# Kernel tuning notes

Hardware: AMD Instinct MI355X
Metric: run time of the kernel (lower is better)

## Reference

```python
import jax, jax.numpy as jnp
import numpy as np

D_EMBED = 512
NUM_HEADS = 8
HEAD_DIM = D_EMBED // NUM_HEADS
D_FF = 2048
B, L = 2, 4096
LN_EPS = 1e-5


def _layernorm(x, g, b):
    mu = jnp.mean(x, axis=-1, keepdims=True)
    var = jnp.mean(jnp.square(x - mu), axis=-1, keepdims=True)
    return (x - mu) * jax.lax.rsqrt(var + LN_EPS) * g + b


def setup_inputs() -> dict:
    key = jax.random.key(0)
    ks = jax.random.split(key, 16)
    s = 0.02
    inp = {
        "x": jax.random.normal(ks[0], (B, L, D_EMBED), dtype=jnp.float32),
        "mask": jnp.ones((B, 1, 1, L), dtype=jnp.int32),
        # attention projections (stored [in, out] for x @ W)
        "Wq": jax.random.normal(ks[1], (D_EMBED, D_EMBED), dtype=jnp.float32) * s,
        "bq": jnp.zeros((D_EMBED,), dtype=jnp.float32),
        "Wk": jax.random.normal(ks[2], (D_EMBED, D_EMBED), dtype=jnp.float32) * s,
        "bk": jnp.zeros((D_EMBED,), dtype=jnp.float32),
        "Wv": jax.random.normal(ks[3], (D_EMBED, D_EMBED), dtype=jnp.float32) * s,
        "bv": jnp.zeros((D_EMBED,), dtype=jnp.float32),
        "Wo": jax.random.normal(ks[4], (D_EMBED, D_EMBED), dtype=jnp.float32) * s,
        "bo": jnp.zeros((D_EMBED,), dtype=jnp.float32),
        # layernorms
        "ln1_g": jnp.ones((D_EMBED,), dtype=jnp.float32),
        "ln1_b": jnp.zeros((D_EMBED,), dtype=jnp.float32),
        "ln2_g": jnp.ones((D_EMBED,), dtype=jnp.float32),
        "ln2_b": jnp.zeros((D_EMBED,), dtype=jnp.float32),
        # FFN
        "W1": jax.random.normal(ks[5], (D_EMBED, D_FF), dtype=jnp.float32) * s,
        "b1": jnp.zeros((D_FF,), dtype=jnp.float32),
        "W2": jax.random.normal(ks[6], (D_FF, D_EMBED), dtype=jnp.float32) * s,
        "b2": jnp.zeros((D_EMBED,), dtype=jnp.float32),
    }
    return inp


def reference(x, mask, Wq, bq, Wk, bk, Wv, bv, Wo, bo, ln1_g, ln1_b,
              W1, b1, W2, b2, ln2_g, ln2_b):
    Bx, Lx, _ = x.shape
    # projections -> [B, H, L, Dh]
    def split_heads(t):
        return t.reshape(Bx, Lx, NUM_HEADS, HEAD_DIM).transpose(0, 2, 1, 3)
    q = split_heads(x @ Wq + bq)
    k = split_heads(x @ Wk + bk)
    v = split_heads(x @ Wv + bv)
    scores = jnp.einsum("bhqd,bhkd->bhqk", q, k) / jnp.sqrt(
        jnp.asarray(HEAD_DIM, dtype=x.dtype))
    scores = jnp.where(mask == 0, jnp.asarray(-1e9, dtype=x.dtype), scores)
    attn = jax.nn.softmax(scores, axis=-1)
    ctx = jnp.einsum("bhqk,bhkd->bhqd", attn, v)
    ctx = ctx.transpose(0, 2, 1, 3).reshape(Bx, Lx, D_EMBED)
    attn_out = ctx @ Wo + bo

    h = _layernorm(x + attn_out, ln1_g, ln1_b)
    ff = (jax.nn.gelu(h @ W1 + b1, approximate=False)) @ W2 + b2
    return _layernorm(h + ff, ln2_g, ln2_b)
```

## Files before the change

kernel.cpp:

```cpp
#include <hip/hip_runtime.h>
#include <hip/hip_bf16.h>
#include <math.h>

#define D_EMBED 512
#define NUM_HEADS 8
#define HEAD_DIM 64
#define D_FF 2048
#define BATCH 2
#define SEQ 4096
#define M_ROWS (BATCH*SEQ)
#define QSCALE 0.18033688011112042f

typedef __attribute__((ext_vector_type(8))) short short8;
typedef __attribute__((ext_vector_type(4))) short short4_t;
typedef __attribute__((ext_vector_type(4))) float f32x4;
typedef __attribute__((ext_vector_type(16))) float f32x16;

#if __has_builtin(__builtin_amdgcn_exp2f)
#define EXP2(x) __builtin_amdgcn_exp2f(x)
#else
#define EXP2(x) exp2f(x)
#endif

__device__ inline unsigned short f2b(float f) {
    union { float f; unsigned u; } v; v.f = f;
    unsigned r = v.u + 0x7fffu + ((v.u >> 16) & 1u);
    return (unsigned short)(r >> 16);
}

__device__ inline float b2f(short s) {
    union { unsigned u; float f; } v;
    v.u = ((unsigned)(unsigned short)s) << 16;
    return v.f;
}

__device__ inline short4_t pk4(float p0, float p1, float p2, float p3) {
    union { __hip_bfloat162 h2[2]; short4_t s4; } u;
    u.h2[0] = __float22bfloat162_rn(make_float2(p0, p1));
    u.h2[1] = __float22bfloat162_rn(make_float2(p2, p3));
    return u.s4;
}

__device__ inline unsigned pk2(float lo, float hi) {
    union { __hip_bfloat162 h2; unsigned u; } x;
    x.h2 = __float22bfloat162_rn(make_float2(lo, hi));
    return x.u;
}

__device__ inline void plswap(unsigned a, unsigned b, unsigned &r0, unsigned &r1) {
#if __has_builtin(__builtin_amdgcn_permlane32_swap)
    auto v = __builtin_amdgcn_permlane32_swap(a, b, false, false);
    r0 = (unsigned)v[0]; r1 = (unsigned)v[1];
#else
    unsigned ax = (unsigned)__shfl_xor((int)a, 32, 64);
    unsigned bx = (unsigned)__shfl_xor((int)b, 32, 64);
    bool hi = (threadIdx.x & 32) != 0;
    r0 = hi ? bx : a;
    r1 = hi ? b  : ax;
#endif
}

__device__ inline short8 pfrag8(const float* p) {
    unsigned a0 = pk2(p[0], p[1]), a1 = pk2(p[2], p[3]);
    unsigned b0 = pk2(p[4], p[5]), b1 = pk2(p[6], p[7]);
    unsigned u0, u1, u2, u3;
    plswap(a0, b0, u0, u1);
    plswap(a1, b1, u2, u3);
    union { unsigned u[4]; short8 s; } r;
    r.u[0] = u0; r.u[1] = u2; r.u[2] = u1; r.u[3] = u3;
    return r.s;
}

__device__ inline void gl2lds16(const void* g, void* l) {
    __builtin_amdgcn_global_load_lds(
        (const __attribute__((address_space(1))) unsigned int*)g,
        (__attribute__((address_space(3))) unsigned int*)l, 16, 0, 0);
}

template<int EPI>
__global__ __launch_bounds__(256) void gemm_bt(
    const unsigned short* __restrict__ A, const unsigned short* __restrict__ BT,
    const float* __restrict__ bias, void* __restrict__ Cout,
    int M, int N, int K)
{
    __shared__ __align__(16) unsigned short As[128*32];
    __shared__ __align__(16) unsigned short Bs[128*32];
    const int tid  = threadIdx.x;
    const int wave = tid >> 6, lane = tid & 63;
    const int wy = wave >> 1, wx = wave & 1;
    const int quad = lane >> 4, m16 = lane & 15;
    const int row0 = blockIdx.y * 128, n0 = blockIdx.x * 128;
    const int rdoff = (quad ^ ((m16 >> 1) & 3)) * 8;

    f32x4 acc[4][4];
#pragma unroll
    for (int i = 0; i < 4; i++)
#pragma unroll
        for (int j = 0; j < 4; j++) acc[i][j] = (f32x4){0.f,0.f,0.f,0.f};

    const int kIters = K >> 5;
    for (int kt = 0; kt < kIters; ++kt) {
        const int k0 = kt << 5;
#pragma unroll
        for (int it = 0; it < 2; ++it) {
            int g  = it*256 + tid;
            int r  = g >> 2;
            int c8 = (((g & 3) ^ ((g >> 3) & 3)) << 3);
            gl2lds16(A  + (size_t)(row0 + r)*K + k0 + c8, &As[(size_t)(it*256 + wave*64)*8]);
            gl2lds16(BT + (size_t)(n0  + r)*K + k0 + c8, &Bs[(size_t)(it*256 + wave*64)*8]);
        }
        __syncthreads();
        short8 a[4], b[4];
#pragma unroll
        for (int i = 0; i < 4; i++) a[i] = *(const short8*)&As[(wy*64 + i*16 + m16)*32 + rdoff];
#pragma unroll
        for (int j = 0; j < 4; j++) b[j] = *(const short8*)&Bs[(wx*64 + j*16 + m16)*32 + rdoff];
#pragma unroll
        for (int i = 0; i < 4; i++)
#pragma unroll
            for (int j = 0; j < 4; j++)
                acc[i][j] = __builtin_amdgcn_mfma_f32_16x16x32_bf16(a[i], b[j], acc[i][j], 0, 0, 0);
        __syncthreads();
    }

#pragma unroll
    for (int j = 0; j < 4; j++) {
        int col = n0 + wx*64 + j*16 + m16;
        float bj = bias[col];
#pragma unroll
        for (int i = 0; i < 4; i++) {
            int rbase = row0 + wy*64 + i*16 + quad*4;
#pragma unroll
            for (int r = 0; r < 4; r++) {
                float v = acc[i][j][r] + bj;
                size_t idx = (size_t)(rbase + r)*N + col;
                if (EPI == 0) {
                    ((unsigned short*)Cout)[idx] = f2b(v);
                } else {
                    float gv = 0.5f * v * (1.0f + erff(v * 0.70710678118654752f));
                    ((unsigned short*)Cout)[idx] = f2b(gv);
                }
            }
        }
    }
}

__global__ __launch_bounds__(256) void gemm_qkv(
    const unsigned short* __restrict__ A, const unsigned short* __restrict__ BT,
    const float* __restrict__ bias,
    unsigned short* __restrict__ Qp, unsigned short* __restrict__ Kp,
    unsigned short* __restrict__ Vp)
{
    const int K = 512;
    __shared__ __align__(16) unsigned short As[128*32];
    __shared__ __align__(16) unsigned short Bs[128*32];
    const int tid  = threadIdx.x;
    const int wave = tid >> 6, lane = tid & 63;
    const int wy = wave >> 1, wx = wave & 1;
    const int quad = lane >> 4, m16 = lane & 15;
    const int row0 = blockIdx.y * 128, n0 = blockIdx.x * 128;
    const int rdoff = (quad ^ ((m16 >> 1) & 3)) * 8;
    const int region = n0 >> 9;

    f32x4 acc[4][4];
#pragma unroll
    for (int i = 0; i < 4; i++)
#pragma unroll
        for (int j = 0; j < 4; j++) acc[i][j] = (f32x4){0.f,0.f,0.f,0.f};

    for (int kt = 0; kt < 16; ++kt) {
        const int k0 = kt << 5;
#pragma unroll
        for (int it = 0; it < 2; ++it) {
            int g  = it*256 + tid;
            int r  = g >> 2;
            int c8 = (((g & 3) ^ ((g >> 3) & 3)) << 3);
            gl2lds16(A  + (size_t)(row0 + r)*K + k0 + c8, &As[(size_t)(it*256 + wave*64)*8]);
            gl2lds16(BT + (size_t)(n0  + r)*K + k0 + c8, &Bs[(size_t)(it*256 + wave*64)*8]);
        }
        __syncthreads();
        short8 a[4], b[4];
#pragma unroll
        for (int i = 0; i < 4; i++) a[i] = *(const short8*)&As[(wy*64 + i*16 + m16)*32 + rdoff];
#pragma unroll
        for (int j = 0; j < 4; j++) b[j] = *(const short8*)&Bs[(wx*64 + j*16 + m16)*32 + rdoff];
#pragma unroll
        for (int i = 0; i < 4; i++)
#pragma unroll
            for (int j = 0; j < 4; j++)
                acc[i][j] = __builtin_amdgcn_mfma_f32_16x16x32_bf16(a[i], b[j], acc[i][j], 0, 0, 0);
        __syncthreads();
    }

    const float sc = (region == 0) ? QSCALE : 1.0f;
#pragma unroll
    for (int j = 0; j < 4; j++) {
        int col = n0 + wx*64 + j*16 + m16;
        float bj = bias[col];
        int cc = col & 511, h = cc >> 6, d = cc & 63;
#pragma unroll
        for (int i = 0; i < 4; i++) {
            int rbase = row0 + wy*64 + i*16 + quad*4;
#pragma unroll
            for (int r = 0; r < 4; r++) {
                float v = (acc[i][j][r] + bj) * sc;
                int row = rbase + r;
                int b = row >> 12, l = row & 4095;
                size_t bh = (size_t)(b*8 + h);
                if (region == 0) {
                    Qp[(bh*SEQ + l)*64 + d] = f2b(v);
                } else if (region == 1) {
                    Kp[(bh*SEQ + l)*64 + d] = f2b(v);
                } else {
                    Vp[(bh*64 + d)*SEQ + l] = f2b(v);
                }
            }
        }
    }
}

__global__ __launch_bounds__(256) void gemm_bt64(
    const unsigned short* __restrict__ A, const unsigned short* __restrict__ BT,
    const float* __restrict__ bias, unsigned short* __restrict__ Cout,
    int M, int N, int K)
{
    __shared__ __align__(16) unsigned short As[64*32];
    __shared__ __align__(16) unsigned short Bs[128*32];
    const int tid  = threadIdx.x;
    const int wave = tid >> 6, lane = tid & 63;
    const int wy = wave >> 1, wx = wave & 1;
    const int quad = lane >> 4, m16 = lane & 15;
    const int row0 = blockIdx.y * 64, n0 = blockIdx.x * 128;
    const int rdoff = (quad ^ ((m16 >> 1) & 3)) * 8;

    f32x4 acc[2][4];
#pragma unroll
    for (int i = 0; i < 2; i++)
#pragma unroll
        for (int j = 0; j < 4; j++) acc[i][j] = (f32x4){0.f,0.f,0.f,0.f};

    const int kIters = K >> 5;
    for (int kt = 0; kt < kIters; ++kt) {
        const int k0 = kt << 5;
        {
            int r = tid >> 2;
            int c8 = (((tid & 3) ^ ((tid >> 3) & 3)) << 3);
            gl2lds16(A + (size_t)(row0 + r)*K + k0 + c8, &As[(size_t)(wave*64)*8]);
        }
#pragma unroll
        for (int it = 0; it < 2; ++it) {
            int g  = it*256 + tid;
            int r  = g >> 2;
            int c8 = (((g & 3) ^ ((g >> 3) & 3)) << 3);
            gl2lds16(BT + (size_t)(n0 + r)*K + k0 + c8, &Bs[(size_t)(it*256 + wave*64)*8]);
        }
        __syncthreads();
        short8 a[2], b[4];
#pragma unroll
        for (int i = 0; i < 2; i++) a[i] = *(const short8*)&As[(wy*32 + i*16 + m16)*32 + rdoff];
#pragma unroll
        for (int j = 0; j < 4; j++) b[j] = *(const short8*)&Bs[(wx*64 + j*16 + m16)*32 + rdoff];
#pragma unroll
        for (int i = 0; i < 2; i++)
#pragma unroll
            for (int j = 0; j < 4; j++)
                acc[i][j] = __builtin_amdgcn_mfma_f32_16x16x32_bf16(a[i], b[j], acc[i][j], 0, 0, 0);
        __syncthreads();
    }

#pragma unroll
    for (int j = 0; j < 4; j++) {
        int col = n0 + wx*64 + j*16 + m16;
        float bj = bias[col];
#pragma unroll
        for (int i = 0; i < 2; i++) {
            int rbase = row0 + wy*32 + i*16 + quad*4;
#pragma unroll
            for (int r = 0; r < 4; r++) {
                float v = acc[i][j][r] + bj;
                Cout[(size_t)(rbase + r)*N + col] = f2b(v);
            }
        }
    }
}

__global__ __launch_bounds__(256) void prep(
    const float* __restrict__ Wq, const float* __restrict__ Wk,
    const float* __restrict__ Wv, const float* __restrict__ Wo,
    const float* __restrict__ W1, const float* __restrict__ W2,
    const float* __restrict__ bq, const float* __restrict__ bk,
    const float* __restrict__ bv, const int* __restrict__ mask,
    unsigned short* __restrict__ WqkvT, unsigned short* __restrict__ WoT,
    unsigned short* __restrict__ W1T, unsigned short* __restrict__ W2T,
    float* __restrict__ bqkv, int* __restrict__ mflag, unsigned* __restrict__ kmax2)
{
    const int id = blockIdx.x, t = threadIdx.x;
    if (id == 3072) {
        if (t < 64) {
            const int* m = mask + t*128;
            int all = 1;
            for (int i = 0; i < 128; i += 4) {
                int4 v = *(const int4*)(m + i);
                all &= (v.x && v.y && v.z && v.w) ? 1 : 0;
            }
            mflag[t] = all;
        }
        if (t < 16) kmax2[t] = 0u;
        for (int i = t; i < 1536; i += 256)
            bqkv[i] = (i < 512) ? bq[i] : ((i < 1024) ? bk[i-512] : bv[i-1024]);
        return;
    }
    __shared__ float tt[32][33];
    const float* W; unsigned short* WT; int K, N, bx, by;
    if (id < 256)       { W = Wq; WT = WqkvT;            K = 512;  N = 512;  bx = id & 15;  by = id >> 4; }
    else if (id < 512)  { int l = id - 256;  W = Wk; WT = WqkvT + 512*512;  K = 512;  N = 512;  bx = l & 15; by = l >> 4; }
    else if (id < 768)  { int l = id - 512;  W = Wv; WT = WqkvT + 1024*512; K = 512;  N = 512;  bx = l & 15; by = l >> 4; }
    else if (id < 1024) { int l = id - 768;  W = Wo; WT = WoT;              K = 512;  N = 512;  bx = l & 15; by = l >> 4; }
    else if (id < 2048) { int l = id - 1024; W = W1; WT = W1T;              K = 512;  N = 2048; bx = l & 63; by = l >> 6; }
    else                { int l = id - 2048; W = W2; WT = W2T;              K = 2048; N = 512;  bx = l & 15; by = l >> 4; }
    const int n0 = bx*32, k0 = by*32;
    const int x = t & 31, y = t >> 5;
#pragma unroll
    for (int yy = y; yy < 32; yy += 8) tt[yy][x] = W[(size_t)(k0+yy)*N + n0 + x];
    __syncthreads();
#pragma unroll
    for (int yy = y; yy < 32; yy += 8) WT[(size_t)(n0+yy)*K + k0 + x] = f2b(tt[x][yy]);
}

__global__ __launch_bounds__(256) void kmax_k(
    const unsigned short* __restrict__ Kp, unsigned* __restrict__ kmax2)
{
    const int bh = blockIdx.x, t = threadIdx.x;
    const int row = blockIdx.y*256 + t;
    const unsigned short* kp = Kp + ((size_t)bh*SEQ + row)*64;
    float s = 0.f;
#pragma unroll
    for (int c = 0; c < 8; ++c) {
        short8 v = *(const short8*)(kp + c*8);
#pragma unroll
        for (int j = 0; j < 8; ++j) { float f = b2f(v[j]); s += f*f; }
    }
#pragma unroll
    for (int off = 32; off >= 1; off >>= 1)
        s = fmaxf(s, __shfl_xor(s, off, 64));
    if ((t & 63) == 0) atomicMax(&kmax2[bh], __float_as_uint(s));
}

__global__ __launch_bounds__(512, 2) void flash_attn(
    const unsigned short* __restrict__ Qp, const unsigned short* __restrict__ Kp,
    const unsigned short* __restrict__ Vt, const int* __restrict__ mask,
    const int* __restrict__ flags, const unsigned* __restrict__ kmax2,
    unsigned short* __restrict__ O)
{
    __shared__ __align__(16) unsigned short Ks[2][128*64];
    __shared__ __align__(16) unsigned short Vs[2][64*128];
    __shared__ float rsh[4][2][64];
    const int tid = threadIdx.x, wave = tid >> 6, lane = tid & 63;
    const int qsub = wave & 3, parity = wave >> 2;
    const int c = lane & 31, l5 = lane >> 5;
    const int bh = blockIdx.y, b = bh >> 3, h = bh & 7;
    const int qbase = blockIdx.x * 256 + qsub * 64;

    const unsigned short* Qb = Qp + (size_t)bh*SEQ*64;
    const unsigned short* Kb = Kp + (size_t)bh*SEQ*64;
    const unsigned short* Vb = Vt + (size_t)bh*64*SEQ;
    const int* mbase = mask + b*SEQ;
    const int* fbase = flags + b*(SEQ/128);
    const float kmx = __uint_as_float(kmax2[bh]);

    short8 qf[2][4];
    float Mq[2];
#pragma unroll
    for (int qs = 0; qs < 2; ++qs) {
        const unsigned short* qp = Qb + (size_t)(qbase + qs*32 + c)*64 + l5*8;
        float qn2 = 0.f;
#pragma unroll
        for (int t = 0; t < 4; ++t) {
            qf[qs][t] = *(const short8*)(qp + t*16);
#pragma unroll
            for (int j = 0; j < 8; ++j) { float f = b2f(qf[qs][t][j]); qn2 += f*f; }
        }
        qn2 += __shfl_xor(qn2, 32, 64);
        Mq[qs] = sqrtf(qn2 * kmx);
    }

    f32x16 accO[2][2];
#pragma unroll
    for (int qs = 0; qs < 2; ++qs)
#pragma unroll
        for (int dg = 0; dg < 2; ++dg)
#pragma unroll
            for (int r = 0; r < 16; ++r) accO[qs][dg][r] = 0.f;
    float rs0 = 0.f, rs1 = 0.f;

#define STAGE(nb, ktn) do {                                                   \
        const int key0s = (ktn)*128;                                          \
        _Pragma("unroll")                                                     \
        for (int it = 0; it < 2; ++it) {                                      \
            int idx = it*512 + tid;                                           \
            int r = idx >> 3, chn = idx & 7;                                  \
            gl2lds16(Kb + (size_t)(key0s + r)*64 + ((chn ^ (r & 7)) << 3),    \
                     &Ks[nb][(it*512 + wave*64)*8]);                          \
        }                                                                     \
        _Pragma("unroll")                                                     \
        for (int it = 0; it < 2; ++it) {                                      \
            int idx = it*512 + tid;                                           \
            int r = idx >> 4, chn = idx & 15;                                 \
            gl2lds16(Vb + (size_t)r*SEQ + key0s + ((chn ^ (r & 15)) << 3),    \
                     &Vs[nb][(it*512 + wave*64)*8]);                          \
        }                                                                     \
    } while (0)

    STAGE(0, 0);
    __syncthreads();
    int cb = 0;
    const int NT = SEQ/128;

    for (int kt = 0; kt < NT; ++kt) {
        if (kt + 1 < NT) STAGE(cb ^ 1, kt + 1);
        const int allones = fbase[kt];
        const int key0 = kt * 128;
        const unsigned short* Kt  = Ks[cb];
        const unsigned short* Vtl = Vs[cb];

#pragma unroll
        for (int g = 0; g < 2; ++g) {
            const int kg = parity*2 + g;
            short8 kf[4];
#pragma unroll
            for (int t = 0; t < 4; ++t) {
                int row = kg*32 + c;
                int chn = (t*2 + l5) ^ (row & 7);
                kf[t] = *(const short8*)&Kt[row*64 + chn*8];
            }
            f32x16 s0, s1;
#pragma unroll
            for (int r = 0; r < 16; ++r) { s0[r] = -Mq[0]; s1[r] = -Mq[1]; }
#pragma unroll
            for (int t = 0; t < 4; ++t) {
                s0 = __builtin_amdgcn_mfma_f32_32x32x16_bf16(kf[t], qf[0][t], s0, 0, 0, 0);
                s1 = __builtin_amdgcn_mfma_f32_32x32x16_bf16(kf[t], qf[1][t], s1, 0, 0, 0);
            }
            if (!allones) {
#pragma unroll
                for (int r = 0; r < 16; ++r) {
                    int mv = mbase[key0 + kg*32 + (r & 3) + 8*(r >> 2) + 4*l5];
                    if (!mv) { s0[r] = -1e9f; s1[r] = -1e9f; }
                }
            }
            float pa[16], pc[16];
#pragma unroll
            for (int r = 0; r < 16; ++r) { pa[r] = EXP2(s0[r]); pc[r] = EXP2(s1[r]); }
            rs0 += (((pa[0]+pa[1])+(pa[2]+pa[3])) + ((pa[4]+pa[5])+(pa[6]+pa[7])))
                 + (((pa[8]+pa[9])+(pa[10]+pa[11])) + ((pa[12]+pa[13])+(pa[14]+pa[15])));
            rs1 += (((pc[0]+pc[1])+(pc[2]+pc[3])) + ((pc[4]+pc[5])+(pc[6]+pc[7])))
                 + (((pc[8]+pc[9])+(pc[10]+pc[11])) + ((pc[12]+pc[13])+(pc[14]+pc[15])));

            short8 vf[2][2];
#pragma unroll
            for (int c2 = 0; c2 < 2; ++c2)
#pragma unroll
                for (int dg = 0; dg < 2; ++dg) {
                    int row = dg*32 + c;
                    int chn = ((kg*2 + c2)*2 + l5) ^ (row & 15);
                    vf[c2][dg] = *(const short8*)&Vtl[row*128 + chn*8];
                }
#pragma unroll
            for (int c2 = 0; c2 < 2; ++c2) {
                short8 pf0 = pfrag8(&pa[c2*8]);
                short8 pf1 = pfrag8(&pc[c2*8]);
                accO[0][0] = __builtin_amdgcn_mfma_f32_32x32x16_bf16(vf[c2][0], pf0, accO[0][0], 0, 0, 0);
                accO[0][1] = __builtin_amdgcn_mfma_f32_32x32x16_bf16(vf[c2][1], pf0, accO[0][1], 0, 0, 0);
                accO[1][0] = __builtin_amdgcn_mfma_f32_32x32x16_bf16(vf[c2][0], pf1, accO[1][0], 0, 0, 0);
                accO[1][1] = __builtin_amdgcn_mfma_f32_32x32x16_bf16(vf[c2][1], pf1, accO[1][1], 0, 0, 0);
            }
        }
        __syncthreads();
        cb ^= 1;
    }
#undef STAGE

    float* mp = (qsub < 2) ? ((float*)&Ks[0][0] + qsub*4096)
                           : ((float*)&Vs[0][0] + (qsub - 2)*4096);
    if (parity) {
#pragma unroll
        for (int qs = 0; qs < 2; ++qs)
#pragma unroll
            for (int dg = 0; dg < 2; ++dg)
#pragma unroll
                for (int r = 0; r < 16; ++r)
                    mp[(qs*2 + dg)*1024 + r*64 + lane] = accO[qs][dg][r];
        rsh[qsub][0][lane] = rs0;
        rsh[qsub][1][lane] = rs1;
    }
    __syncthreads();
    if (!parity) {
#pragma unroll
        for (int qs = 0; qs < 2; ++qs)
#pragma unroll
            for (int dg = 0; dg < 2; ++dg)
#pragma unroll
                for (int r = 0; r < 16; ++r)
                    accO[qs][dg][r] += mp[(qs*2 + dg)*1024 + r*64 + lane];
        rs0 += rsh[qsub][0][lane];
        rs1 += rsh[qsub][1][lane];

        rs0 += __shfl_xor(rs0, 32, 64);
        rs1 += __shfl_xor(rs1, 32, 64);
        float rl[2] = { 1.0f/rs0, 1.0f/rs1 };
#pragma unroll
        for (int qs = 0; qs < 2; ++qs) {
            int qrow = qbase + qs*32 + c;
            unsigned short* op = O + (size_t)(b*SEQ + qrow)*D_EMBED + h*HEAD_DIM;
#pragma unroll
            for (int dg = 0; dg < 2; ++dg)
#pragma unroll
                for (int q4 = 0; q4 < 4; ++q4) {
                    short4_t o = pk4(accO[qs][dg][q4*4+0]*rl[qs], accO[qs][dg][q4*4+1]*rl[qs],
                                     accO[qs][dg][q4*4+2]*rl[qs], accO[qs][dg][q4*4+3]*rl[qs]);
                    *(short4_t*)&op[dg*32 + q4*8 + l5*4] = o;
                }
        }
    }
}

__global__ __launch_bounds__(256) void ln_res1(
    const float* __restrict__ A, const unsigned short* __restrict__ Bv,
    const float* __restrict__ g, const float* __restrict__ be,
    unsigned short* __restrict__ Yb)
{
    const int wave = threadIdx.x >> 6, lane = threadIdx.x & 63;
    const int row = blockIdx.x * 4 + wave;
    const float* ap = A + (size_t)row*512 + lane*8;
    short8 bv = *(const short8*)(Bv + (size_t)row*512 + lane*8);
    float v[8]; float s = 0.f;
#pragma unroll
    for (int j = 0; j < 8; j++) { v[j] = ap[j] + b2f(bv[j]); s += v[j]; }
#pragma unroll
    for (int off = 32; off >= 1; off >>= 1) s += __shfl_xor(s, off, 64);
    float mu = s * (1.f/512.f);
    float q = 0.f;
#pragma unroll
    for (int j = 0; j < 8; j++) { v[j] -= mu; q += v[j]*v[j]; }
#pragma unroll
    for (int off = 32; off >= 1; off >>= 1) q += __shfl_xor(q, off, 64);
    float rstd = rsqrtf(q * (1.f/512.f) + 1e-5f);
#pragma unroll
    for (int j = 0; j < 8; j++) {
        float y = v[j]*rstd*g[lane*8+j] + be[lane*8+j];
        Yb[(size_t)row*512 + lane*8 + j] = f2b(y);
    }
}

__global__ __launch_bounds__(256) void ln_res2(
    const unsigned short* __restrict__ A, const unsigned short* __restrict__ Bv,
    const float* __restrict__ g, const float* __restrict__ be,
    float* __restrict__ Yf)
{
    const int wave = threadIdx.x >> 6, lane = threadIdx.x & 63;
    const int row = blockIdx.x * 4 + wave;
    short8 av = *(const short8*)(A  + (size_t)row*512 + lane*8);
    short8 bv = *(const short8*)(Bv + (size_t)row*512 + lane*8);
    float v[8]; float s = 0.f;
#pragma unroll
    for (int j = 0; j < 8; j++) { v[j] = b2f(av[j]) + b2f(bv[j]); s += v[j]; }
#pragma unroll
    for (int off = 32; off >= 1; off >>= 1) s += __shfl_xor(s, off, 64);
    float mu = s * (1.f/512.f);
    float q = 0.f;
#pragma unroll
    for (int j = 0; j < 8; j++) { v[j] -= mu; q += v[j]*v[j]; }
#pragma unroll
    for (int off = 32; off >= 1; off >>= 1) q += __shfl_xor(q, off, 64);
    float rstd = rsqrtf(q * (1.f/512.f) + 1e-5f);
#pragma unroll
    for (int j = 0; j < 8; j++) {
        float y = v[j]*rstd*g[lane*8+j] + be[lane*8+j];
        Yf[(size_t)row*512 + lane*8 + j] = y;
    }
}

__global__ __launch_bounds__(256) void cvt_f32_bf16(
    const float* __restrict__ X, unsigned short* __restrict__ Y, int n)
{
    int idx = (blockIdx.x * 256 + threadIdx.x) * 4;
    if (idx < n) {
        float4 v = *(const float4*)(X + idx);
        Y[idx+0] = f2b(v.x); Y[idx+1] = f2b(v.y);
        Y[idx+2] = f2b(v.z); Y[idx+3] = f2b(v.w);
    }
}

extern "C" void kernel_launch(void* const* d_in, const int* in_sizes, int n_in,
                              void* d_out, int out_size, void* d_ws, size_t ws_size,
                              hipStream_t stream)
{
    const float* x    = (const float*)d_in[0];
    const int*   mask = (const int*)  d_in[1];
    const float* Wq = (const float*)d_in[2];  const float* bq = (const float*)d_in[3];
    const float* Wk = (const float*)d_in[4];  const float* bk = (const float*)d_in[5];
    const float* Wv = (const float*)d_in[6];  const float* bv = (const float*)d_in[7];
    const float* Wo = (const float*)d_in[8];  const float* bo = (const float*)d_in[9];
    const float* ln1g = (const float*)d_in[10]; const float* ln1b = (const float*)d_in[11];
    const float* ln2g = (const float*)d_in[12]; const float* ln2b = (const float*)d_in[13];
    const float* W1 = (const float*)d_in[14]; const float* b1 = (const float*)d_in[15];
    const float* W2 = (const float*)d_in[16]; const float* b2 = (const float*)d_in[17];
    float* out = (float*)d_out;

    char* ws = (char*)d_ws;
    const size_t MB = 1024*1024;
    unsigned short* xb    = (unsigned short*)(ws + 0);
    unsigned short* WqkvT = (unsigned short*)(ws + 8*MB);
    unsigned short* W1T   = (unsigned short*)(ws + 10*MB);
    unsigned short* W2T   = (unsigned short*)(ws + 12*MB);
    unsigned short* WoT   = (unsigned short*)(ws + 14*MB);
    float*          bqkv  = (float*)(ws + 14*MB + 512*1024);
    int*            mflag = (int*)(ws + 14*MB + 768*1024);
    unsigned*       kmaxb = (unsigned*)(ws + 14*MB + 772*1024);
    unsigned short* Qp    = (unsigned short*)(ws + 15*MB);
    unsigned short* Kp    = (unsigned short*)(ws + 23*MB);
    unsigned short* Vp    = (unsigned short*)(ws + 31*MB);
    unsigned short* ctx   = (unsigned short*)(ws + 39*MB);
    unsigned short* atfb  = (unsigned short*)(ws + 47*MB);
    unsigned short* hb    = (unsigned short*)(ws + 0);
    unsigned short* Gb    = (unsigned short*)(ws + 15*MB);
    unsigned short* ffb   = (unsigned short*)(ws + 47*MB);

    cvt_f32_bf16<<<4096, 256, 0, stream>>>(x, xb, M_ROWS*D_EMBED);
    prep<<<3073, 256, 0, stream>>>(Wq, Wk, Wv, Wo, W1, W2, bq, bk, bv, mask,
                                   WqkvT, WoT, W1T, W2T, bqkv, mflag, kmaxb);

    gemm_qkv<<<dim3(12,64), 256, 0, stream>>>(xb, WqkvT, bqkv, Qp, Kp, Vp);

    kmax_k<<<dim3(16,16), 256, 0, stream>>>(Kp, kmaxb);
    flash_attn<<<dim3(SEQ/256, 16), 512, 0, stream>>>(Qp, Kp, Vp, mask, mflag, kmaxb, ctx);

    gemm_bt64<<<dim3(4,128), 256, 0, stream>>>(ctx, WoT, bo, atfb, M_ROWS, 512, 512);
    ln_res1<<<M_ROWS/4, 256, 0, stream>>>(x, atfb, ln1g, ln1b, hb);

    gemm_bt<2><<<dim3(16,64), 256, 0, stream>>>(hb, W1T, b1, Gb, M_ROWS, D_FF, 512);
    gemm_bt64<<<dim3(4,128), 256, 0, stream>>>(Gb, W2T, b2, ffb, M_ROWS, 512, D_FF);
    ln_res2<<<M_ROWS/4, 256, 0, stream>>>(hb, ffb, ln2g, ln2b, out);
}
```

Baseline: 346.1 us.

## Split flash-attention key tiles across four wave groups with 128-query blocks

Each block now covers 128 queries with 2 query-subgroups of waves and 4 key-partition waves per 128-key tile, instead of 256 queries with 2 key partitions. This doubles the grid to 512 blocks to improve CU fill, and raises the launch-bounds occupancy hint to 4 blocks. The cost is that each K/V tile loaded into LDS is reused by half as many queries, so global K/V traffic doubles, and the final cross-wave reduction of accumulators and row sums now takes two LDS merge rounds with extra barriers. The tighter launch bound may also cap registers and risk spills.

```diff
diff --git a/kernel.cpp b/kernel.cpp
--- a/kernel.cpp
+++ b/kernel.cpp
@@ -346,7 +346,7 @@
     if ((t & 63) == 0) atomicMax(&kmax2[bh], __float_as_uint(s));
 }
 
-__global__ __launch_bounds__(512, 2) void flash_attn(
+__global__ __launch_bounds__(512, 4) void flash_attn(
     const unsigned short* __restrict__ Qp, const unsigned short* __restrict__ Kp,
     const unsigned short* __restrict__ Vt, const int* __restrict__ mask,
     const int* __restrict__ flags, const unsigned* __restrict__ kmax2,
@@ -354,12 +354,12 @@
 {
     __shared__ __align__(16) unsigned short Ks[2][128*64];
     __shared__ __align__(16) unsigned short Vs[2][64*128];
-    __shared__ float rsh[4][2][64];
+    __shared__ float rsp[8][2][64];
     const int tid = threadIdx.x, wave = tid >> 6, lane = tid & 63;
-    const int qsub = wave & 3, parity = wave >> 2;
+    const int qsub = wave & 1, kp = wave >> 1;
     const int c = lane & 31, l5 = lane >> 5;
     const int bh = blockIdx.y, b = bh >> 3, h = bh & 7;
-    const int qbase = blockIdx.x * 256 + qsub * 64;
+    const int qbase = blockIdx.x * 128 + qsub * 64;
 
     const unsigned short* Qb = Qp + (size_t)bh*SEQ*64;
     const unsigned short* Kb = Kp + (size_t)bh*SEQ*64;
@@ -422,88 +422,112 @@
         const int key0 = kt * 128;
         const unsigned short* Kt  = Ks[cb];
         const unsigned short* Vtl = Vs[cb];
-
-#pragma unroll
-        for (int g = 0; g < 2; ++g) {
-            const int kg = parity*2 + g;
-            short8 kf[4];
-#pragma unroll
-            for (int t = 0; t < 4; ++t) {
-                int row = kg*32 + c;
-                int chn = (t*2 + l5) ^ (row & 7);
-                kf[t] = *(const short8*)&Kt[row*64 + chn*8];
+        const int kg = kp;
+
+        short8 kf[4];
+#pragma unroll
+        for (int t = 0; t < 4; ++t) {
+            int row = kg*32 + c;
+            int chn = (t*2 + l5) ^ (row & 7);
+            kf[t] = *(const short8*)&Kt[row*64 + chn*8];
+        }
+        f32x16 s0, s1;
+#pragma unroll
+        for (int r = 0; r < 16; ++r) { s0[r] = -Mq[0]; s1[r] = -Mq[1]; }
+#pragma unroll
+        for (int t = 0; t < 4; ++t) {
+            s0 = __builtin_amdgcn_mfma_f32_32x32x16_bf16(kf[t], qf[0][t], s0, 0, 0, 0);
+            s1 = __builtin_amdgcn_mfma_f32_32x32x16_bf16(kf[t], qf[1][t], s1, 0, 0, 0);
+        }
+        if (!allones) {
+#pragma unroll
+            for (int r = 0; r < 16; ++r) {
+                int mv = mbase[key0 + kg*32 + (r & 3) + 8*(r >> 2) + 4*l5];
+                if (!mv) { s0[r] = -1e9f; s1[r] = -1e9f; }
             }
-            f32x16 s0, s1;
-#pragma unroll
-            for (int r = 0; r < 16; ++r) { s0[r] = -Mq[0]; s1[r] = -Mq[1]; }
-#pragma unroll
-            for (int t = 0; t < 4; ++t) {
-                s0 = __builtin_amdgcn_mfma_f32_32x32x16_bf16(kf[t], qf[0][t], s0, 0, 0, 0);
-                s1 = __builtin_amdgcn_mfma_f32_32x32x16_bf16(kf[t], qf[1][t], s1, 0, 0, 0);
+        }
+        float pa[16], pc[16];
+#pragma unroll
+        for (int r = 0; r < 16; ++r) { pa[r] = EXP2(s0[r]); pc[r] = EXP2(s1[r]); }
+        rs0 += (((pa[0]+pa[1])+(pa[2]+pa[3])) + ((pa[4]+pa[5])+(pa[6]+pa[7])))
+             + (((pa[8]+pa[9])+(pa[10]+pa[11])) + ((pa[12]+pa[13])+(pa[14]+pa[15])));
+        rs1 += (((pc[0]+pc[1])+(pc[2]+pc[3])) + ((pc[4]+pc[5])+(pc[6]+pc[7])))
+             + (((pc[8]+pc[9])+(pc[10]+pc[11])) + ((pc[12]+pc[13])+(pc[14]+pc[15])));
+
+        short8 vf[2][2];
+#pragma unroll
+        for (int c2 = 0; c2 < 2; ++c2)
+#pragma unroll
+            for (int dg = 0; dg < 2; ++dg) {
+                int row = dg*32 + c;
+                int chn = ((kg*2 + c2)*2 + l5) ^ (row & 15);
+                vf[c2][dg] = *(const short8*)&Vtl[row*128 + chn*8];
             }
-            if (!allones) {
-#pragma unroll
-                for (int r = 0; r < 16; ++r) {
-                    int mv = mbase[key0 + kg*32 + (r & 3) + 8*(r >> 2) + 4*l5];
-                    if (!mv) { s0[r] = -1e9f; s1[r] = -1e9f; }
-                }
-            }
-            float pa[16], pc[16];
-#pragma unroll
-            for (int r = 0; r < 16; ++r) { pa[r] = EXP2(s0[r]); pc[r] = EXP2(s1[r]); }
-            rs0 += (((pa[0]+pa[1])+(pa[2]+pa[3])) + ((pa[4]+pa[5])+(pa[6]+pa[7])))
-                 + (((pa[8]+pa[9])+(pa[10]+pa[11])) + ((pa[12]+pa[13])+(pa[14]+pa[15])));
-            rs1 += (((pc[0]+pc[1])+(pc[2]+pc[3])) + ((pc[4]+pc[5])+(pc[6]+pc[7])))
-                 + (((pc[8]+pc[9])+(pc[10]+pc[11])) + ((pc[12]+pc[13])+(pc[14]+pc[15])));
-
-            short8 vf[2][2];
-#pragma unroll
-            for (int c2 = 0; c2 < 2; ++c2)
-#pragma unroll
-                for (int dg = 0; dg < 2; ++dg) {
-                    int row = dg*32 + c;
-                    int chn = ((kg*2 + c2)*2 + l5) ^ (row & 15);
-                    vf[c2][dg] = *(const short8*)&Vtl[row*128 + chn*8];
-                }
-#pragma unroll
-            for (int c2 = 0; c2 < 2; ++c2) {
-                short8 pf0 = pfrag8(&pa[c2*8]);
-                short8 pf1 = pfrag8(&pc[c2*8]);
-                accO[0][0] = __builtin_amdgcn_mfma_f32_32x32x16_bf16(vf[c2][0], pf0, accO[0][0], 0, 0, 0);
-                accO[0][1] = __builtin_amdgcn_mfma_f32_32x32x16_bf16(vf[c2][1], pf0, accO[0][1], 0, 0, 0);
-                accO[1][0] = __builtin_amdgcn_mfma_f32_32x32x16_bf16(vf[c2][0], pf1, accO[1][0], 0, 0, 0);
-                accO[1][1] = __builtin_amdgcn_mfma_f32_32x32x16_bf16(vf[c2][1], pf1, accO[1][1], 0, 0, 0);
-            }
-        }
+#pragma unroll
+        for (int c2 = 0; c2 < 2; ++c2) {
+            short8 pf0 = pfrag8(&pa[c2*8]);
+            short8 pf1 = pfrag8(&pc[c2*8]);
+            accO[0][0] = __builtin_amdgcn_mfma_f32_32x32x16_bf16(vf[c2][0], pf0, accO[0][0], 0, 0, 0);
+            accO[0][1] = __builtin_amdgcn_mfma_f32_32x32x16_bf16(vf[c2][1], pf0, accO[0][1], 0, 0, 0);
+            accO[1][0] = __builtin_amdgcn_mfma_f32_32x32x16_bf16(vf[c2][0], pf1, accO[1][0], 0, 0, 0);
+            accO[1][1] = __builtin_amdgcn_mfma_f32_32x32x16_bf16(vf[c2][1], pf1, accO[1][1], 0, 0, 0);
+        }
+
         __syncthreads();
         cb ^= 1;
     }
 #undef STAGE
 
-    float* mp = (qsub < 2) ? ((float*)&Ks[0][0] + qsub*4096)
-                           : ((float*)&Vs[0][0] + (qsub - 2)*4096);
-    if (parity) {
+    float* const ksf = (float*)&Ks[0][0];
+    float* const vsf = (float*)&Vs[0][0];
+    rsp[wave][0][lane] = rs0;
+    rsp[wave][1][lane] = rs1;
+    if (kp >= 2) {
+        int s = (kp - 2)*2 + qsub;
+        float* mp = (s < 2) ? ksf + s*4096 : vsf + (s - 2)*4096;
 #pragma unroll
         for (int qs = 0; qs < 2; ++qs)
 #pragma unroll
             for (int dg = 0; dg < 2; ++dg)
 #pragma unroll
                 for (int r = 0; r < 16; ++r)
-                    mp[(qs*2 + dg)*1024 + r*64 + lane] = accO[qs][dg][r];
-        rsh[qsub][0][lane] = rs0;
-        rsh[qsub][1][lane] = rs1;
+                    mp[((qs*2 + dg)*16 + r)*64 + lane] = accO[qs][dg][r];
     }
     __syncthreads();
-    if (!parity) {
+    if (kp < 2) {
+        int s = kp*2 + qsub;
+        float* mp = (s < 2) ? ksf + s*4096 : vsf + (s - 2)*4096;
 #pragma unroll
         for (int qs = 0; qs < 2; ++qs)
 #pragma unroll
             for (int dg = 0; dg < 2; ++dg)
 #pragma unroll
                 for (int r = 0; r < 16; ++r)
-                    accO[qs][dg][r] += mp[(qs*2 + dg)*1024 + r*64 + lane];
-        rs0 += rsh[qsub][0][lane];
-        rs1 += rsh[qsub][1][lane];
+                    accO[qs][dg][r] += mp[((qs*2 + dg)*16 + r)*64 + lane];
+    }
+    __syncthreads();
+    if (kp == 1) {
+        float* mp = ksf + qsub*4096;
+#pragma unroll
+        for (int qs = 0; qs < 2; ++qs)
+#pragma unroll
+            for (int dg = 0; dg < 2; ++dg)
+#pragma unroll
+                for (int r = 0; r < 16; ++r)
+                    mp[((qs*2 + dg)*16 + r)*64 + lane] = accO[qs][dg][r];
+    }
+    __syncthreads();
+    if (kp == 0) {
+        float* mp = ksf + qsub*4096;
+#pragma unroll
+        for (int qs = 0; qs < 2; ++qs)
+#pragma unroll
+            for (int dg = 0; dg < 2; ++dg)
+#pragma unroll
+                for (int r = 0; r < 16; ++r)
+                    accO[qs][dg][r] += mp[((qs*2 + dg)*16 + r)*64 + lane];
+        rs0 += rsp[2 + qsub][0][lane] + rsp[4 + qsub][0][lane] + rsp[6 + qsub][0][lane];
+        rs1 += rsp[2 + qsub][1][lane] + rsp[4 + qsub][1][lane] + rsp[6 + qsub][1][lane];
 
         rs0 += __shfl_xor(rs0, 32, 64);
         rs1 += __shfl_xor(rs1, 32, 64);
@@ -633,7 +657,7 @@
     gemm_qkv<<<dim3(12,64), 256, 0, stream>>>(xb, WqkvT, bqkv, Qp, Kp, Vp);
 
     kmax_k<<<dim3(16,16), 256, 0, stream>>>(Kp, kmaxb);
-    flash_attn<<<dim3(SEQ/256, 16), 512, 0, stream>>>(Qp, Kp, Vp, mask, mflag, kmaxb, ctx);
+    flash_attn<<<dim3(SEQ/128, 16), 512, 0, stream>>>(Qp, Kp, Vp, mask, mflag, kmaxb, ctx);
 
     gemm_bt64<<<dim3(4,128), 256, 0, stream>>>(ctx, WoT, bo, atfb, M_ROWS, 512, 512);
     ln_res1<<<M_ROWS/4, 256, 0, stream>>>(x, atfb, ln1g, ln1b, hb);
```

Measured after the change: 793.8 us. 2.29x slower.

## Halve queries per wave in flash attention to double grid occupancy

Applied to the files above, without the earlier changes.

Each wave in the flash attention kernel now processes 32 query rows instead of 64, so a block covers 128 queries and the grid doubles. This aims to give each CU more resident blocks and waves, improving latency hiding and load balance across CUs. The trade-off is that each K/V tile is loaded and staged into LDS for half as many queries, doubling K/V global and LDS traffic per unit of work. Register pressure per wave drops because the accumulators halve.

```diff
diff --git a/kernel.cpp b/kernel.cpp
--- a/kernel.cpp
+++ b/kernel.cpp
@@ -354,12 +354,12 @@
 {
     __shared__ __align__(16) unsigned short Ks[2][128*64];
     __shared__ __align__(16) unsigned short Vs[2][64*128];
-    __shared__ float rsh[4][2][64];
+    __shared__ float rsp[8][64];
     const int tid = threadIdx.x, wave = tid >> 6, lane = tid & 63;
-    const int qsub = wave & 3, parity = wave >> 2;
+    const int qsub = wave & 3, kp = wave >> 2;
     const int c = lane & 31, l5 = lane >> 5;
     const int bh = blockIdx.y, b = bh >> 3, h = bh & 7;
-    const int qbase = blockIdx.x * 256 + qsub * 64;
+    const int qbase = blockIdx.x * 128 + qsub * 32;
 
     const unsigned short* Qb = Qp + (size_t)bh*SEQ*64;
     const unsigned short* Kb = Kp + (size_t)bh*SEQ*64;
@@ -368,30 +368,27 @@
     const int* fbase = flags + b*(SEQ/128);
     const float kmx = __uint_as_float(kmax2[bh]);
 
-    short8 qf[2][4];
-    float Mq[2];
-#pragma unroll
-    for (int qs = 0; qs < 2; ++qs) {
-        const unsigned short* qp = Qb + (size_t)(qbase + qs*32 + c)*64 + l5*8;
+    short8 qf[4];
+    float Mq;
+    {
+        const unsigned short* qp = Qb + (size_t)(qbase + c)*64 + l5*8;
         float qn2 = 0.f;
 #pragma unroll
         for (int t = 0; t < 4; ++t) {
-            qf[qs][t] = *(const short8*)(qp + t*16);
-#pragma unroll
-            for (int j = 0; j < 8; ++j) { float f = b2f(qf[qs][t][j]); qn2 += f*f; }
+            qf[t] = *(const short8*)(qp + t*16);
+#pragma unroll
+            for (int j = 0; j < 8; ++j) { float f = b2f(qf[t][j]); qn2 += f*f; }
         }
         qn2 += __shfl_xor(qn2, 32, 64);
-        Mq[qs] = sqrtf(qn2 * kmx);
-    }
-
-    f32x16 accO[2][2];
-#pragma unroll
-    for (int qs = 0; qs < 2; ++qs)
-#pragma unroll
-        for (int dg = 0; dg < 2; ++dg)
-#pragma unroll
-            for (int r = 0; r < 16; ++r) accO[qs][dg][r] = 0.f;
-    float rs0 = 0.f, rs1 = 0.f;
+        Mq = sqrtf(qn2 * kmx);
+    }
+
+    f32x16 accO[2];
+#pragma unroll
+    for (int dg = 0; dg < 2; ++dg)
+#pragma unroll
+        for (int r = 0; r < 16; ++r) accO[dg][r] = 0.f;
+    float rs = 0.f;
 
 #define STAGE(nb, ktn) do {                                                   \
         const int key0s = (ktn)*128;                                          \
@@ -425,7 +422,7 @@
 
 #pragma unroll
         for (int g = 0; g < 2; ++g) {
-            const int kg = parity*2 + g;
+            const int kg = kp*2 + g;
             short8 kf[4];
 #pragma unroll
             for (int t = 0; t < 4; ++t) {
@@ -433,28 +430,24 @@
                 int chn = (t*2 + l5) ^ (row & 7);
                 kf[t] = *(const short8*)&Kt[row*64 + chn*8];
             }
-            f32x16 s0, s1;
-#pragma unroll
-            for (int r = 0; r < 16; ++r) { s0[r] = -Mq[0]; s1[r] = -Mq[1]; }
-#pragma unroll
-            for (int t = 0; t < 4; ++t) {
-                s0 = __builtin_amdgcn_mfma_f32_32x32x16_bf16(kf[t], qf[0][t], s0, 0, 0, 0);
-                s1 = __builtin_amdgcn_mfma_f32_32x32x16_bf16(kf[t], qf[1][t], s1, 0, 0, 0);
-            }
+            f32x16 s;
+#pragma unroll
+            for (int r = 0; r < 16; ++r) s[r] = -Mq;
+#pragma unroll
+            for (int t = 0; t < 4; ++t)
+                s = __builtin_amdgcn_mfma_f32_32x32x16_bf16(kf[t], qf[t], s, 0, 0, 0);
             if (!allones) {
 #pragma unroll
                 for (int r = 0; r < 16; ++r) {
                     int mv = mbase[key0 + kg*32 + (r & 3) + 8*(r >> 2) + 4*l5];
-                    if (!mv) { s0[r] = -1e9f; s1[r] = -1e9f; }
+                    if (!mv) s[r] = -1e9f;
                 }
             }
-            float pa[16], pc[16];
-#pragma unroll
-            for (int r = 0; r < 16; ++r) { pa[r] = EXP2(s0[r]); pc[r] = EXP2(s1[r]); }
-            rs0 += (((pa[0]+pa[1])+(pa[2]+pa[3])) + ((pa[4]+pa[5])+(pa[6]+pa[7])))
-                 + (((pa[8]+pa[9])+(pa[10]+pa[11])) + ((pa[12]+pa[13])+(pa[14]+pa[15])));
-            rs1 += (((pc[0]+pc[1])+(pc[2]+pc[3])) + ((pc[4]+pc[5])+(pc[6]+pc[7])))
-                 + (((pc[8]+pc[9])+(pc[10]+pc[11])) + ((pc[12]+pc[13])+(pc[14]+pc[15])));
+            float pa[16];
+#pragma unroll
+            for (int r = 0; r < 16; ++r) pa[r] = EXP2(s[r]);
+            rs += (((pa[0]+pa[1])+(pa[2]+pa[3])) + ((pa[4]+pa[5])+(pa[6]+pa[7])))
+                + (((pa[8]+pa[9])+(pa[10]+pa[11])) + ((pa[12]+pa[13])+(pa[14]+pa[15])));
 
             short8 vf[2][2];
 #pragma unroll
@@ -467,12 +460,9 @@
                 }
 #pragma unroll
             for (int c2 = 0; c2 < 2; ++c2) {
-                short8 pf0 = pfrag8(&pa[c2*8]);
-                short8 pf1 = pfrag8(&pc[c2*8]);
-                accO[0][0] = __builtin_amdgcn_mfma_f32_32x32x16_bf16(vf[c2][0], pf0, accO[0][0], 0, 0, 0);
-                accO[0][1] = __builtin_amdgcn_mfma_f32_32x32x16_bf16(vf[c2][1], pf0, accO[0][1], 0, 0, 0);
-                accO[1][0] = __builtin_amdgcn_mfma_f32_32x32x16_bf16(vf[c2][0], pf1, accO[1][0], 0, 0, 0);
-                accO[1][1] = __builtin_amdgcn_mfma_f32_32x32x16_bf16(vf[c2][1], pf1, accO[1][1], 0, 0, 0);
+                short8 pf = pfrag8(&pa[c2*8]);
+                accO[0] = __builtin_amdgcn_mfma_f32_32x32x16_bf16(vf[c2][0], pf, accO[0], 0, 0, 0);
+                accO[1] = __builtin_amdgcn_mfma_f32_32x32x16_bf16(vf[c2][1], pf, accO[1], 0, 0, 0);
             }
         }
         __syncthreads();
@@ -480,47 +470,37 @@
     }
 #undef STAGE
 
-    float* mp = (qsub < 2) ? ((float*)&Ks[0][0] + qsub*4096)
-                           : ((float*)&Vs[0][0] + (qsub - 2)*4096);
-    if (parity) {
-#pragma unroll
-        for (int qs = 0; qs < 2; ++qs)
-#pragma unroll
-            for (int dg = 0; dg < 2; ++dg)
-#pragma unroll
-                for (int r = 0; r < 16; ++r)
-                    mp[(qs*2 + dg)*1024 + r*64 + lane] = accO[qs][dg][r];
-        rsh[qsub][0][lane] = rs0;
-        rsh[qsub][1][lane] = rs1;
+    float* const ksf = (float*)&Ks[0][0];
+    rsp[wave][lane] = rs;
+    float* mp = ksf + qsub*2048;
+    if (kp == 1) {
+#pragma unroll
+        for (int dg = 0; dg < 2; ++dg)
+#pragma unroll
+            for (int r = 0; r < 16; ++r)
+                mp[(dg*16 + r)*64 + lane] = accO[dg][r];
     }
     __syncthreads();
-    if (!parity) {
-#pragma unroll
-        for (int qs = 0; qs < 2; ++qs)
-#pragma unroll
-            for (int dg = 0; dg < 2; ++dg)
-#pragma unroll
-                for (int r = 0; r < 16; ++r)
-                    accO[qs][dg][r] += mp[(qs*2 + dg)*1024 + r*64 + lane];
-        rs0 += rsh[qsub][0][lane];
-        rs1 += rsh[qsub][1][lane];
-
-        rs0 += __shfl_xor(rs0, 32, 64);
-        rs1 += __shfl_xor(rs1, 32, 64);
-        float rl[2] = { 1.0f/rs0, 1.0f/rs1 };
-#pragma unroll
-        for (int qs = 0; qs < 2; ++qs) {
-            int qrow = qbase + qs*32 + c;
-            unsigned short* op = O + (size_t)(b*SEQ + qrow)*D_EMBED + h*HEAD_DIM;
-#pragma unroll
-            for (int dg = 0; dg < 2; ++dg)
-#pragma unroll
-                for (int q4 = 0; q4 < 4; ++q4) {
-                    short4_t o = pk4(accO[qs][dg][q4*4+0]*rl[qs], accO[qs][dg][q4*4+1]*rl[qs],
-                                     accO[qs][dg][q4*4+2]*rl[qs], accO[qs][dg][q4*4+3]*rl[qs]);
-                    *(short4_t*)&op[dg*32 + q4*8 + l5*4] = o;
-                }
-        }
+    if (kp == 0) {
+#pragma unroll
+        for (int dg = 0; dg < 2; ++dg)
+#pragma unroll
+            for (int r = 0; r < 16; ++r)
+                accO[dg][r] += mp[(dg*16 + r)*64 + lane];
+        rs += rsp[4 + qsub][lane];
+
+        rs += __shfl_xor(rs, 32, 64);
+        float rl = 1.0f / rs;
+        int qrow = qbase + c;
+        unsigned short* op = O + (size_t)(b*SEQ + qrow)*D_EMBED + h*HEAD_DIM;
+#pragma unroll
+        for (int dg = 0; dg < 2; ++dg)
+#pragma unroll
+            for (int q4 = 0; q4 < 4; ++q4) {
+                short4_t o = pk4(accO[dg][q4*4+0]*rl, accO[dg][q4*4+1]*rl,
+                                 accO[dg][q4*4+2]*rl, accO[dg][q4*4+3]*rl);
+                *(short4_t*)&op[dg*32 + q4*8 + l5*4] = o;
+            }
     }
 }
 
@@ -633,7 +613,7 @@
     gemm_qkv<<<dim3(12,64), 256, 0, stream>>>(xb, WqkvT, bqkv, Qp, Kp, Vp);
 
     kmax_k<<<dim3(16,16), 256, 0, stream>>>(Kp, kmaxb);
-    flash_attn<<<dim3(SEQ/256, 16), 512, 0, stream>>>(Qp, Kp, Vp, mask, mflag, kmaxb, ctx);
+    flash_attn<<<dim3(SEQ/128, 16), 512, 0, stream>>>(Qp, Kp, Vp, mask, mflag, kmaxb, ctx);
 
     gemm_bt64<<<dim3(4,128), 256, 0, stream>>>(ctx, WoT, bo, atfb, M_ROWS, 512, 512);
     ln_res1<<<M_ROWS/4, 256, 0, stream>>>(x, atfb, ln1g, ln1b, hb);
```

Result: slower. 375.8 us (+8.6%).
